# Kernel optimization log

Hardware: AMD Instinct MI355X
Metric: run time of the kernel (lower is better)

The kernel has to match this reference:

```python
import jax, jax.numpy as jnp
import numpy as np

SEQ, BATCH, D_IN, D_H = 512, 64, 1024, 1024


def setup_inputs() -> dict:
    key = jax.random.key(0)
    ks = jax.random.split(key, 5)
    scale_ih = 1.0 / np.sqrt(D_IN)
    scale_hh = 1.0 / np.sqrt(D_H)
    return {
        "x": jax.random.normal(ks[0], (SEQ, BATCH, D_IN), dtype=jnp.float32),
        "h0": jnp.zeros((BATCH, D_H), dtype=jnp.float32),
        "W_ih": jax.random.normal(ks[1], (D_H, D_IN), dtype=jnp.float32) * scale_ih,
        "b_ih": jax.random.normal(ks[2], (D_H,), dtype=jnp.float32) * scale_ih,
        "W_hh": jax.random.normal(ks[3], (D_H, D_H), dtype=jnp.float32) * scale_hh,
        "b_hh": jax.random.normal(ks[4], (D_H,), dtype=jnp.float32) * scale_hh,
    }


def reference(x, h0, W_ih, b_ih, W_hh, b_hh):
    # Elman RNN: h_t = tanh(x_t @ W_ih^T + b_ih + h_{t-1} @ W_hh^T + b_hh)
    # Input projection has no time dependency -> one big batched GEMM.
    x_proj = jnp.einsum("sbi,hi->sbh", x, W_ih) + b_ih + b_hh  # [S, B, H]

    def step(h_prev, xp_t):
        h_t = jnp.tanh(xp_t + h_prev @ W_hh.T)
        return h_t, h_t

    h_last, output = jax.lax.scan(step, h0, x_proj)
    return output, h_last  # ([S, B, H], [B, H])
```

## Files before the change

kernel.cpp:

```cpp
#include <hip/hip_runtime.h>
#include <hip/hip_cooperative_groups.h>
#include <cmath>

namespace cg = cooperative_groups;

#define SEQ   512
#define BATCH 64
#define DIN   1024
#define DH    1024

typedef float f4 __attribute__((ext_vector_type(4)));

__global__ __launch_bounds__(256) void proj_kernel(
    const float* __restrict__ X, const float* __restrict__ W,
    const float* __restrict__ b_ih, const float* __restrict__ b_hh,
    float* __restrict__ C) {
  __shared__ float As[64][17];
  __shared__ float Bs[64][17];
  const int m0 = blockIdx.x * 64;
  const int n0 = blockIdx.y * 64;
  const int tid = threadIdx.x;
  const int tm = tid >> 4;
  const int tn = tid & 15;
  const int lrow = tid >> 2;
  const int lk4  = (tid & 3) * 4;

  float acc[4][4];
#pragma unroll
  for (int i = 0; i < 4; ++i)
#pragma unroll
    for (int j = 0; j < 4; ++j) acc[i][j] = 0.f;

  for (int kt = 0; kt < DIN; kt += 16) {
    float4 av = *(const float4*)(X + (size_t)(m0 + lrow) * DIN + kt + lk4);
    float4 bv = *(const float4*)(W + (size_t)(n0 + lrow) * DIN + kt + lk4);
    __syncthreads();
    As[lrow][lk4 + 0] = av.x; As[lrow][lk4 + 1] = av.y;
    As[lrow][lk4 + 2] = av.z; As[lrow][lk4 + 3] = av.w;
    Bs[lrow][lk4 + 0] = bv.x; Bs[lrow][lk4 + 1] = bv.y;
    Bs[lrow][lk4 + 2] = bv.z; Bs[lrow][lk4 + 3] = bv.w;
    __syncthreads();
#pragma unroll
    for (int kk = 0; kk < 16; ++kk) {
      float a[4], b[4];
#pragma unroll
      for (int i = 0; i < 4; ++i) a[i] = As[tm * 4 + i][kk];
#pragma unroll
      for (int j = 0; j < 4; ++j) b[j] = Bs[tn * 4 + j][kk];
#pragma unroll
      for (int i = 0; i < 4; ++i)
#pragma unroll
        for (int j = 0; j < 4; ++j) acc[i][j] += a[i] * b[j];
    }
  }

#pragma unroll
  for (int j = 0; j < 4; ++j) {
    const int n = n0 + tn * 4 + j;
    const float bias = b_ih[n] + b_hh[n];
#pragma unroll
    for (int i = 0; i < 4; ++i) {
      const int m = m0 + tm * 4 + i;
      C[(size_t)m * DH + n] = acc[i][j] + bias;
    }
  }
}

__global__ __launch_bounds__(256) void transpose_h0(
    const float* __restrict__ h0, float* __restrict__ hT, unsigned* cnt) {
  const int idx = blockIdx.x * 256 + threadIdx.x;
  const int k4 = idx >> 6;
  const int b = idx & 63;
  float4 v = *(const float4*)(h0 + (size_t)b * DH + (k4 << 2));
  ((float4*)hT)[idx] = v;
  if (cnt != nullptr && blockIdx.x == 0 && threadIdx.x < 160) {
    __hip_atomic_store(&cnt[threadIdx.x], 0u, __ATOMIC_RELAXED,
                       __HIP_MEMORY_SCOPE_AGENT);
  }
}

__global__ __launch_bounds__(1024, 4) void rnn_fast(
    const float* __restrict__ W_hh, float* __restrict__ out,
    float* __restrict__ hA, float* __restrict__ hB, unsigned* cnt) {
  __shared__ float red[4 * 1093];
  const int tid = threadIdx.x;
  const int bx = blockIdx.x;
  const int b = tid & 63;
  const int wv = tid >> 6;
  const int j0 = __builtin_amdgcn_readfirstlane(bx << 2);
  const float* __restrict__ w0 = W_hh + (size_t)j0 * DH;
  const float* __restrict__ w1 = w0 + DH;
  const float* __restrict__ w2 = w1 + DH;
  const float* __restrict__ w3 = w2 + DH;
  const int kq4 = __builtin_amdgcn_readfirstlane(wv << 4);
  const int fjj = tid & 3;
  const int fb  = tid >> 2;
  unsigned* leaf = cnt + ((bx & 7) << 4);
  unsigned* root = cnt + 128;
  unsigned* flag = cnt + 144;
  int sense = 1;
  bool dead = false;

  for (int t = 0; t < SEQ; ++t) {
    const f4* __restrict__ hp4 = (const f4*)((t & 1) ? hB : hA);
    float* __restrict__ hn = (t & 1) ? hA : hB;
    const f4* pb = hp4 + (kq4 << 6) + b;

    f4 q0, q1, q2, q3, q4, q5, q6, q7, q8, q9, q10, q11, q12, q13, q14, q15;
#define LQ(i) asm volatile("global_load_dwordx4 %0, %1, off sc0 sc1" \
                           : "=v"(q##i) : "v"(pb + ((i) << 6)) : "memory");
    LQ(0)  LQ(1)  LQ(2)  LQ(3)  LQ(4)  LQ(5)  LQ(6)  LQ(7)
    LQ(8)  LQ(9)  LQ(10) LQ(11) LQ(12) LQ(13) LQ(14) LQ(15)
#undef LQ

    size_t ob = 0;
    float xp = 0.f;
    if (tid < 256) {
      ob = ((size_t)t * BATCH + fb) * DH + j0 + fjj;
      xp = out[ob];
    }

    asm volatile("s_waitcnt vmcnt(0)"
                 : "+v"(q0), "+v"(q1), "+v"(q2), "+v"(q3),
                   "+v"(q4), "+v"(q5), "+v"(q6), "+v"(q7),
                   "+v"(q8), "+v"(q9), "+v"(q10), "+v"(q11),
                   "+v"(q12), "+v"(q13), "+v"(q14), "+v"(q15)
                 :: "memory");

    float a0 = 0.f, a1 = 0.f, a2 = 0.f, a3 = 0.f;
#define CH(Q, c) { \
    const int k = (kq4 + (c)) << 2; \
    a0 = fmaf(w0[k + 0], Q.x, a0); a1 = fmaf(w1[k + 0], Q.x, a1); \
    a2 = fmaf(w2[k + 0], Q.x, a2); a3 = fmaf(w3[k + 0], Q.x, a3); \
    a0 = fmaf(w0[k + 1], Q.y, a0); a1 = fmaf(w1[k + 1], Q.y, a1); \
    a2 = fmaf(w2[k + 1], Q.y, a2); a3 = fmaf(w3[k + 1], Q.y, a3); \
    a0 = fmaf(w0[k + 2], Q.z, a0); a1 = fmaf(w1[k + 2], Q.z, a1); \
    a2 = fmaf(w2[k + 2], Q.z, a2); a3 = fmaf(w3[k + 2], Q.z, a3); \
    a0 = fmaf(w0[k + 3], Q.w, a0); a1 = fmaf(w1[k + 3], Q.w, a1); \
    a2 = fmaf(w2[k + 3], Q.w, a2); a3 = fmaf(w3[k + 3], Q.w, a3); \
  }
    CH(q0, 0)   CH(q1, 1)   CH(q2, 2)   CH(q3, 3)
    CH(q4, 4)   CH(q5, 5)   CH(q6, 6)   CH(q7, 7)
    CH(q8, 8)   CH(q9, 9)   CH(q10, 10) CH(q11, 11)
    CH(q12, 12) CH(q13, 13) CH(q14, 14) CH(q15, 15)
#undef CH

    red[0 * 1093 + b * 17 + wv] = a0;
    red[1 * 1093 + b * 17 + wv] = a1;
    red[2 * 1093 + b * 17 + wv] = a2;
    red[3 * 1093 + b * 17 + wv] = a3;
    __syncthreads();

    if (tid < 256) {
      float s = 0.f;
#pragma unroll
      for (int u = 0; u < 16; ++u) s += red[fjj * 1093 + fb * 17 + u];
      const float v = tanhf(xp + s);
      out[ob] = v;
      float* dst = hn + ((size_t)bx << 8) + tid;
      asm volatile("global_store_dword %0, %1, off sc0 sc1"
                   :: "v"(dst), "v"(v) : "memory");
      if (t == SEQ - 1) {
        float* hl = out + (size_t)SEQ * BATCH * DH;
        hl[(size_t)fb * DH + j0 + fjj] = v;
      }
    }

    asm volatile("s_waitcnt vmcnt(0)" ::: "memory");
    __syncthreads();
    if (!dead && tid == 0) {
      unsigned old = __hip_atomic_fetch_add(leaf, 1u, __ATOMIC_RELAXED,
                                            __HIP_MEMORY_SCOPE_AGENT);
      if (old == 31u) {
        __hip_atomic_store(leaf, 0u, __ATOMIC_RELAXED,
                           __HIP_MEMORY_SCOPE_AGENT);
        asm volatile("s_waitcnt vmcnt(0)" ::: "memory");
        unsigned rold = __hip_atomic_fetch_add(root, 1u, __ATOMIC_RELAXED,
                                               __HIP_MEMORY_SCOPE_AGENT);
        if (rold == 7u) {
          __hip_atomic_store(root, 0u, __ATOMIC_RELAXED,
                             __HIP_MEMORY_SCOPE_AGENT);
          asm volatile("s_waitcnt vmcnt(0)" ::: "memory");
          __hip_atomic_store(flag, (unsigned)sense, __ATOMIC_RELAXED,
                             __HIP_MEMORY_SCOPE_AGENT);
        }
      }
      int guard = 0;
      while (__hip_atomic_load(flag, __ATOMIC_RELAXED,
                               __HIP_MEMORY_SCOPE_AGENT) != (unsigned)sense) {
        __builtin_amdgcn_s_sleep(1);
        if (++guard > (1 << 20)) { dead = true; break; }
      }
    }
    sense ^= 1;
    __syncthreads();
  }
}

__device__ __forceinline__ void rnn_step_body(
    float (*red)[4][64], const float4* __restrict__ hp,
    float* __restrict__ hn, const float* __restrict__ W_hh,
    float* __restrict__ out, int t, int bx, int tid) {
  const int b = tid & 63;
  const int wv = tid >> 6;
  const int j0 = __builtin_amdgcn_readfirstlane(bx << 2);
  const float* __restrict__ w0 = W_hh + (size_t)j0 * DH;
  const float* __restrict__ w1 = w0 + DH;
  const float* __restrict__ w2 = w1 + DH;
  const float* __restrict__ w3 = w2 + DH;
  const int kq4 = __builtin_amdgcn_readfirstlane(wv << 4);
  const int fjj = tid & 3;
  const int fb  = tid >> 2;

  const float4 q0  = hp[((kq4 +  0) << 6) + b];
  const float4 q1  = hp[((kq4 +  1) << 6) + b];
  const float4 q2  = hp[((kq4 +  2) << 6) + b];
  const float4 q3  = hp[((kq4 +  3) << 6) + b];
  const float4 q4  = hp[((kq4 +  4) << 6) + b];
  const float4 q5  = hp[((kq4 +  5) << 6) + b];
  const float4 q6  = hp[((kq4 +  6) << 6) + b];
  const float4 q7  = hp[((kq4 +  7) << 6) + b];
  const float4 q8  = hp[((kq4 +  8) << 6) + b];
  const float4 q9  = hp[((kq4 +  9) << 6) + b];
  const float4 q10 = hp[((kq4 + 10) << 6) + b];
  const float4 q11 = hp[((kq4 + 11) << 6) + b];
  const float4 q12 = hp[((kq4 + 12) << 6) + b];
  const float4 q13 = hp[((kq4 + 13) << 6) + b];
  const float4 q14 = hp[((kq4 + 14) << 6) + b];
  const float4 q15 = hp[((kq4 + 15) << 6) + b];

  size_t ob = 0;
  float xp = 0.f;
  if (tid < 256) {
    ob = ((size_t)t * BATCH + fb) * DH + j0 + fjj;
    xp = out[ob];
  }

  float a0 = 0.f, a1 = 0.f, a2 = 0.f, a3 = 0.f;
#define CH(Q, c) { \
    const int k = (kq4 + (c)) << 2; \
    a0 = fmaf(w0[k + 0], Q.x, a0); a1 = fmaf(w1[k + 0], Q.x, a1); \
    a2 = fmaf(w2[k + 0], Q.x, a2); a3 = fmaf(w3[k + 0], Q.x, a3); \
    a0 = fmaf(w0[k + 1], Q.y, a0); a1 = fmaf(w1[k + 1], Q.y, a1); \
    a2 = fmaf(w2[k + 1], Q.y, a2); a3 = fmaf(w3[k + 1], Q.y, a3); \
    a0 = fmaf(w0[k + 2], Q.z, a0); a1 = fmaf(w1[k + 2], Q.z, a1); \
    a2 = fmaf(w2[k + 2], Q.z, a2); a3 = fmaf(w3[k + 2], Q.z, a3); \
    a0 = fmaf(w0[k + 3], Q.w, a0); a1 = fmaf(w1[k + 3], Q.w, a1); \
    a2 = fmaf(w2[k + 3], Q.w, a2); a3 = fmaf(w3[k + 3], Q.w, a3); \
  }
  CH(q0, 0)   CH(q1, 1)   CH(q2, 2)   CH(q3, 3)
  CH(q4, 4)   CH(q5, 5)   CH(q6, 6)   CH(q7, 7)
  CH(q8, 8)   CH(q9, 9)   CH(q10, 10) CH(q11, 11)
  CH(q12, 12) CH(q13, 13) CH(q14, 14) CH(q15, 15)
#undef CH

  red[wv][0][b] = a0; red[wv][1][b] = a1;
  red[wv][2][b] = a2; red[wv][3][b] = a3;
  __syncthreads();

  if (tid < 256) {
    float s = 0.f;
#pragma unroll
    for (int u = 0; u < 16; ++u) s += red[u][fjj][fb];
    const float v = tanhf(xp + s);
    out[ob] = v;
    hn[((size_t)bx << 8) + tid] = v;
    if (t == SEQ - 1) {
      float* hl = out + (size_t)SEQ * BATCH * DH;
      hl[(size_t)fb * DH + j0 + fjj] = v;
    }
  }
}

__global__ __launch_bounds__(1024) void rnn_persistent_cg(
    const float* __restrict__ W_hh, float* __restrict__ out,
    float* __restrict__ hA, float* __restrict__ hB) {
  __shared__ float red[16][4][64];
  cg::grid_group grid = cg::this_grid();
  const int tid = threadIdx.x;
  const int bx = blockIdx.x;
  for (int t = 0; t < SEQ; ++t) {
    const float4* hp = (const float4*)((t & 1) ? hB : hA);
    float* hn = (t & 1) ? hA : hB;
    rnn_step_body(red, hp, hn, W_hh, out, t, bx, tid);
    grid.sync();
  }
}

__global__ __launch_bounds__(1024) void rnn_step_kernel(
    const float* __restrict__ hTprev, float* __restrict__ hTnext,
    const float* __restrict__ W_hh, float* __restrict__ out, int t) {
  __shared__ float red[16][4][64];
  rnn_step_body(red, (const float4*)hTprev, hTnext, W_hh, out, t,
                blockIdx.x, threadIdx.x);
}

extern "C" void kernel_launch(void* const* d_in, const int* in_sizes, int n_in,
                              void* d_out, int out_size, void* d_ws,
                              size_t ws_size, hipStream_t stream) {
  const float* x    = (const float*)d_in[0];
  const float* h0   = (const float*)d_in[1];
  const float* W_ih = (const float*)d_in[2];
  const float* b_ih = (const float*)d_in[3];
  const float* W_hh = (const float*)d_in[4];
  const float* b_hh = (const float*)d_in[5];
  float* out = (float*)d_out;
  float* hA = (float*)d_ws;
  float* hB = hA + (size_t)DH * BATCH;
  unsigned* cnt = (unsigned*)(hB + (size_t)DH * BATCH);
  const bool fast_ok =
      ws_size >= (size_t)2 * DH * BATCH * sizeof(float) + 1024;

  hipLaunchKernelGGL(proj_kernel, dim3(512, 16), dim3(256), 0, stream,
                     x, W_ih, b_ih, b_hh, out);
  hipLaunchKernelGGL(transpose_h0, dim3(64), dim3(256), 0, stream, h0, hA,
                     fast_ok ? cnt : (unsigned*)nullptr);

  const float* W_hh_p = W_hh;
  float* out_p = out;
  float* hA_p = hA;
  float* hB_p = hB;
  unsigned* cnt_p = cnt;
  hipError_t err = hipErrorUnknown;
  if (fast_ok) {
    void* args[] = {(void*)&W_hh_p, (void*)&out_p, (void*)&hA_p,
                    (void*)&hB_p, (void*)&cnt_p};
    err = hipLaunchCooperativeKernel(reinterpret_cast<void*>(rnn_fast),
                                     dim3(256), dim3(1024), args, 0, stream);
  }
  if (err != hipSuccess) {
    void* args2[] = {(void*)&W_hh_p, (void*)&out_p, (void*)&hA_p,
                     (void*)&hB_p};
    err = hipLaunchCooperativeKernel(
        reinterpret_cast<void*>(rnn_persistent_cg), dim3(256), dim3(1024),
        args2, 0, stream);
  }
  if (err != hipSuccess) {
    for (int t = 0; t < SEQ; ++t) {
      const float* src = (t & 1) ? hB : hA;
      float* dst = (t & 1) ? hA : hB;
      hipLaunchKernelGGL(rnn_step_kernel, dim3(256), dim3(1024), 0, stream,
                         src, dst, W_hh, out, t);
    }
  }
}
```

Baseline: 5.957 ms.

## Replicate hidden-state buffer across eight padded copies to spread read contention

The persistent RNN kernel now writes each new hidden value to eight replicas of the hidden-state buffer, padded with an odd stride, and each block reads from the replica chosen by its block index. All 256 blocks read the full hidden state every step with cache-bypassing loads, so the intent is to spread those reads across more memory channels and cache slices instead of concentrating them on one copy. The cost is eight times the cache-bypassing stores per step and a larger workspace requirement, which may force a fallback path if the workspace is too small.

```diff
diff --git a/kernel.cpp b/kernel.cpp
--- a/kernel.cpp
+++ b/kernel.cpp
@@ -8,6 +8,12 @@
 #define BATCH 64
 #define DIN   1024
 #define DH    1024
+
+#define NREP   8
+#define HS4    16657
+#define HSF    (HS4 * 4)
+#define PS4    (NREP * HS4)
+#define PSF    (PS4 * 4)
 
 typedef float f4 __attribute__((ext_vector_type(4)));
 
@@ -67,12 +73,14 @@
 }
 
 __global__ __launch_bounds__(256) void transpose_h0(
-    const float* __restrict__ h0, float* __restrict__ hT, unsigned* cnt) {
+    const float* __restrict__ h0, float* __restrict__ hb, unsigned* cnt,
+    int R) {
   const int idx = blockIdx.x * 256 + threadIdx.x;
   const int k4 = idx >> 6;
   const int b = idx & 63;
   float4 v = *(const float4*)(h0 + (size_t)b * DH + (k4 << 2));
-  ((float4*)hT)[idx] = v;
+  float4* h4 = (float4*)hb;
+  for (int r = 0; r < R; ++r) h4[(size_t)r * HS4 + idx] = v;
   if (cnt != nullptr && blockIdx.x == 0 && threadIdx.x < 160) {
     __hip_atomic_store(&cnt[threadIdx.x], 0u, __ATOMIC_RELAXED,
                        __HIP_MEMORY_SCOPE_AGENT);
@@ -81,7 +89,7 @@
 
 __global__ __launch_bounds__(1024, 4) void rnn_fast(
     const float* __restrict__ W_hh, float* __restrict__ out,
-    float* __restrict__ hA, float* __restrict__ hB, unsigned* cnt) {
+    float* __restrict__ hb, unsigned* cnt) {
   __shared__ float red[4 * 1093];
   const int tid = threadIdx.x;
   const int bx = blockIdx.x;
@@ -95,6 +103,7 @@
   const int kq4 = __builtin_amdgcn_readfirstlane(wv << 4);
   const int fjj = tid & 3;
   const int fb  = tid >> 2;
+  const int rep = __builtin_amdgcn_readfirstlane(bx & (NREP - 1));
   unsigned* leaf = cnt + ((bx & 7) << 4);
   unsigned* root = cnt + 128;
   unsigned* flag = cnt + 144;
@@ -102,8 +111,9 @@
   bool dead = false;
 
   for (int t = 0; t < SEQ; ++t) {
-    const f4* __restrict__ hp4 = (const f4*)((t & 1) ? hB : hA);
-    float* __restrict__ hn = (t & 1) ? hA : hB;
+    const f4* __restrict__ hp4 =
+        (const f4*)hb + ((t & 1) ? PS4 : 0) + (size_t)rep * HS4;
+    float* __restrict__ hn = hb + ((t & 1) ? 0 : PSF);
     const f4* pb = hp4 + (kq4 << 6) + b;
 
     f4 q0, q1, q2, q3, q4, q5, q6, q7, q8, q9, q10, q11, q12, q13, q14, q15;
@@ -158,8 +168,11 @@
       const float v = tanhf(xp + s);
       out[ob] = v;
       float* dst = hn + ((size_t)bx << 8) + tid;
-      asm volatile("global_store_dword %0, %1, off sc0 sc1"
-                   :: "v"(dst), "v"(v) : "memory");
+#pragma unroll
+      for (int r = 0; r < NREP; ++r) {
+        asm volatile("global_store_dword %0, %1, off sc0 sc1"
+                     :: "v"(dst + (size_t)r * HSF), "v"(v) : "memory");
+      }
       if (t == SEQ - 1) {
         float* hl = out + (size_t)SEQ * BATCH * DH;
         hl[(size_t)fb * DH + j0 + fjj] = v;
@@ -305,30 +318,31 @@
   const float* W_hh = (const float*)d_in[4];
   const float* b_hh = (const float*)d_in[5];
   float* out = (float*)d_out;
-  float* hA = (float*)d_ws;
-  float* hB = hA + (size_t)DH * BATCH;
-  unsigned* cnt = (unsigned*)(hB + (size_t)DH * BATCH);
-  const bool fast_ok =
-      ws_size >= (size_t)2 * DH * BATCH * sizeof(float) + 1024;
+  unsigned* cnt = (unsigned*)d_ws;
+  float* hb = (float*)d_ws + 256;
+  const size_t need = 1024 + (size_t)2 * NREP * HSF * sizeof(float);
+  const bool fast_ok = ws_size >= need;
+  const bool fb_ok = ws_size >= 1024 + (size_t)2 * DH * BATCH * sizeof(float);
 
   hipLaunchKernelGGL(proj_kernel, dim3(512, 16), dim3(256), 0, stream,
                      x, W_ih, b_ih, b_hh, out);
-  hipLaunchKernelGGL(transpose_h0, dim3(64), dim3(256), 0, stream, h0, hA,
-                     fast_ok ? cnt : (unsigned*)nullptr);
+  hipLaunchKernelGGL(transpose_h0, dim3(64), dim3(256), 0, stream, h0, hb,
+                     fast_ok ? cnt : (unsigned*)nullptr, fast_ok ? NREP : 1);
 
   const float* W_hh_p = W_hh;
   float* out_p = out;
-  float* hA_p = hA;
-  float* hB_p = hB;
+  float* hb_p = hb;
+  float* hA_p = hb;
+  float* hB_p = hb + (size_t)DH * BATCH;
   unsigned* cnt_p = cnt;
   hipError_t err = hipErrorUnknown;
   if (fast_ok) {
-    void* args[] = {(void*)&W_hh_p, (void*)&out_p, (void*)&hA_p,
-                    (void*)&hB_p, (void*)&cnt_p};
+    void* args[] = {(void*)&W_hh_p, (void*)&out_p, (void*)&hb_p,
+                    (void*)&cnt_p};
     err = hipLaunchCooperativeKernel(reinterpret_cast<void*>(rnn_fast),
                                      dim3(256), dim3(1024), args, 0, stream);
   }
-  if (err != hipSuccess) {
+  if (err != hipSuccess && fb_ok) {
     void* args2[] = {(void*)&W_hh_p, (void*)&out_p, (void*)&hA_p,
                      (void*)&hB_p};
     err = hipLaunchCooperativeKernel(
@@ -337,8 +351,8 @@
   }
   if (err != hipSuccess) {
     for (int t = 0; t < SEQ; ++t) {
-      const float* src = (t & 1) ? hB : hA;
-      float* dst = (t & 1) ? hA : hB;
+      const float* src = (t & 1) ? hB_p : hA_p;
+      float* dst = (t & 1) ? hA_p : hB_p;
       hipLaunchKernelGGL(rnn_step_kernel, dim3(256), dim3(1024), 0, stream,
                          src, dst, W_hh, out, t);
     }
```

New measurement: 6.187 ms. 1.04x slower.
